# Optimization experiments

Measured on AMD Instinct MI355X. Metric: run time of the kernel, lower is better.

## Reference

```python
import jax, jax.numpy as jnp
import numpy as np

B, Hc, Wc, C, NH, SR, WS = 4, 64, 64, 256, 8, 2, 4
N = Hc * Wc


def _window_partition(x, ws, H, W):
    # x: (B, h, N, d) -> (B*h*nWin, ws*ws, d)
    Bb, h, _, d = x.shape
    x = x.reshape(Bb * h, H // ws, ws, W // ws, ws, d)
    x = x.transpose(0, 1, 3, 2, 4, 5)
    return x.reshape(-1, ws * ws, d)


def _window_reverse(win, ws, H, W, head):
    nwin = (H // ws) * (W // ws)
    Bh = win.shape[0] // nwin
    x = win.reshape(Bh, H // ws, W // ws, ws, ws, -1).transpose(0, 1, 3, 2, 4, 5).reshape(Bh, H, W, -1)
    Bb = Bh // head
    x = x.reshape(Bb, head, H, W, -1).transpose(0, 2, 3, 1, 4)  # heads interleave into channels
    return x.reshape(Bb, H * W, -1)


def _layernorm(x, w, b):
    m = x.mean(-1, keepdims=True)
    v = x.var(-1, keepdims=True)
    return (x - m) / jnp.sqrt(v + 1e-5) * w + b


def setup_inputs() -> dict:
    key = jax.random.key(0)
    ks = jax.random.split(key, 16)
    lin = lambda k, i, o: 0.02 * jax.random.normal(k, (i, o), jnp.float32)
    inp = {
        'x': jax.random.normal(ks[0], (B, N, C), jnp.float32),
        'q1_w': lin(ks[1], C, C // 2), 'q1_b': jnp.zeros((C // 2,), jnp.float32),
        'kv1_w': lin(ks[2], C, C), 'kv1_b': jnp.zeros((C,), jnp.float32),
        'q2_w': lin(ks[3], C, C // 2), 'q2_b': jnp.zeros((C // 2,), jnp.float32),
        'kv2_w': lin(ks[4], C, C), 'kv2_b': jnp.zeros((C,), jnp.float32),
        'lepe_w': lin(ks[5], C, C), 'lepe_b': jnp.zeros((C,), jnp.float32),
        'lepe_conv_w': jnp.sqrt(2.0 / 9.0) * jax.random.normal(ks[6], (C, 1, 3, 3), jnp.float32),
        'lepe_conv_b': jnp.zeros((C,), jnp.float32),
        'sr_w': jnp.sqrt(2.0 / (SR * SR * C)) * jax.random.normal(ks[7], (C, C, SR, SR), jnp.float32),
        'sr_b': jnp.zeros((C,), jnp.float32),
        'norm_w': jnp.ones((C,), jnp.float32), 'norm_b': jnp.zeros((C,), jnp.float32),
        'proj_w': lin(ks[8], C, C), 'proj_b': jnp.zeros((C,), jnp.float32),
        'H': Hc, 'W': Wc,
    }
    return inp


def reference(x, q1_w, q1_b, kv1_w, kv1_b, q2_w, q2_b, kv2_w, kv2_b,
              lepe_w, lepe_b, lepe_conv_w, lepe_conv_b, sr_w, sr_b,
              norm_w, norm_b, proj_w, proj_b, H, W):
    Bb, Nn, Cc = x.shape
    h2 = NH // 2
    d = Cc // NH
    sr = sr_w.shape[-1]
    scale = d ** -0.5
    ws = WS

    # lepe: linear -> depthwise 3x3 conv
    l = (x @ lepe_w + lepe_b).transpose(0, 2, 1).reshape(Bb, Cc, H, W)
    l = jax.lax.conv_general_dilated(l, lepe_conv_w, (1, 1), ((1, 1), (1, 1)),
                                     dimension_numbers=('NCHW', 'OIHW', 'NCHW'),
                                     feature_group_count=Cc) + lepe_conv_b[None, :, None, None]
    lepe = l.reshape(Bb, Cc, Nn).transpose(0, 2, 1)

    # branch 1: spatial-reduction global attention
    q1 = (x @ q1_w + q1_b).reshape(Bb, Nn, h2, d).transpose(0, 2, 1, 3)
    x_img = x.transpose(0, 2, 1).reshape(Bb, Cc, H, W)
    xs = jax.lax.conv_general_dilated(x_img, sr_w, (sr, sr), 'VALID',
                                      dimension_numbers=('NCHW', 'OIHW', 'NCHW')) + sr_b[None, :, None, None]
    N1 = (H // sr) * (W // sr)
    xs = xs.reshape(Bb, Cc, N1).transpose(0, 2, 1)
    xs = jax.nn.gelu(_layernorm(xs, norm_w, norm_b), approximate=False)
    kv1 = (xs @ kv1_w + kv1_b).reshape(Bb, N1, 2, h2, d).transpose(2, 0, 3, 1, 4)
    k1, v1 = kv1[0], kv1[1]
    attn1 = jax.nn.softmax(jnp.einsum('bhnd,bhmd->bhnm', q1, k1) * scale, axis=-1)
    x1 = jnp.einsum('bhnm,bhmd->bnhd', attn1, v1).reshape(Bb, Nn, Cc // 2)
    g = jax.lax.stop_gradient(attn1).mean(1).mean(1).reshape(Bb, H // sr, W // sr)
    g = jnp.repeat(jnp.repeat(g, sr, axis=1), sr, axis=2)  # nearest upsample to (B,H,W)

    # branch 2: Swin-style windowed attention (window 4)
    q2 = (x @ q2_w + q2_b).reshape(Bb, Nn, h2, d).transpose(0, 2, 1, 3)
    kv2 = (x @ kv2_w + kv2_b).reshape(Bb, Nn, 2, h2, d).transpose(2, 0, 3, 1, 4)
    k2, v2 = kv2[0], kv2[1]
    q2w = _window_partition(q2, ws, H, W)
    k2w = _window_partition(k2, ws, H, W)
    v2w = _window_partition(v2, ws, H, W)
    attn2 = jax.nn.softmax(jnp.einsum('wnd,wmd->wnm', q2w, k2w) * scale, axis=-1)
    x2 = jnp.einsum('wnm,wmd->wnd', attn2, v2w)
    x2 = _window_reverse(x2, ws, H, W, h2)
    nwin = (H // ws) * (W // ws)
    lm = jax.lax.stop_gradient(attn2).reshape(Bb, h2, nwin, ws * ws, ws * ws).mean(1).mean(2)
    lm = lm.reshape(Bb, H // ws, W // ws, ws, ws).transpose(0, 1, 3, 2, 4).reshape(Bb, H, W)

    out = jnp.concatenate([x1, x2], axis=-1)
    p = (out + lepe) @ proj_w + proj_b
    out = p + p  # proj_drop is identity at p=0.0, so x = drop(p) + p = 2p

    mask = lm + g
    mask1 = mask.reshape(Bb, H * W)
    mask2 = mask.transpose(0, 2, 1).reshape(Bb, H * W)
    return out, mask1, mask2
```

## Files before the change

kernel.cpp:

```cpp
#include <hip/hip_runtime.h>
#include <hip/hip_bf16.h>
#include <math.h>

typedef __hip_bfloat16 bf16;
typedef __attribute__((ext_vector_type(8))) short bf16x8;
typedef __attribute__((ext_vector_type(4))) short bf16x4;
typedef __attribute__((ext_vector_type(4))) float f32x4;

__device__ __forceinline__ float b2f(bf16 v) { return __bfloat162float(v); }
__device__ __forceinline__ bf16  f2b(float v) { return __float2bfloat16(v); }
__device__ __forceinline__ float s2f(short v) { return __uint_as_float(((unsigned)(unsigned short)v) << 16); }

__global__ void detect_dtype(const void* x, int* flag)
{
    __shared__ int cnt;
    if (threadIdx.x == 0) cnt = 0;
    __syncthreads();
    const unsigned* w = (const unsigned*)x;
    int sane = 0;
    for (int i = threadIdx.x; i < 2048; i += 256) {
        unsigned lo = (w[i] & 0xFFFFu) << 16;
        float v = __uint_as_float(lo);
        float a = fabsf(v);
        if (v == 0.f || (a > 1e-8f && a < 1e4f)) sane++;
    }
    atomicAdd(&cnt, sane);
    __syncthreads();
    if (threadIdx.x == 0) *flag = (cnt < 1640) ? 1 : 0;
}

__global__ void convert_x4(const void* __restrict__ src, bf16* __restrict__ dst,
                           const int* __restrict__ flag)
{
    int i = blockIdx.x * 256 + threadIdx.x;
    bf16 tmp[4];
    if (*flag) {
        float4 v = ((const float4*)src)[i];
        tmp[0] = f2b(v.x); tmp[1] = f2b(v.y); tmp[2] = f2b(v.z); tmp[3] = f2b(v.w);
        *(bf16x4*)&dst[i * 4] = *(bf16x4*)tmp;
    } else {
        ((bf16x4*)dst)[i] = ((const bf16x4*)src)[i];
    }
}

struct PackArgs { const void* src[10]; bf16* dst[10]; int n[10]; };
__global__ void pack_small(PackArgs a, const int* __restrict__ flag)
{
    int bi = blockIdx.x;
    int n = a.n[bi];
    const void* s = a.src[bi];
    bf16* d = a.dst[bi];
    for (int i = threadIdx.x; i < n; i += 256)
        d[i] = (*flag) ? f2b(((const float*)s)[i]) : f2b(s2f(((const short*)s)[i]));
}

struct WTArgs { const void* src[6]; bf16* dst[6]; int N[6]; int blkoff[7]; };
__global__ void convert_wT_multi(WTArgs a, const int* __restrict__ flag)
{
    int blk = blockIdx.x;
    int ti = 0;
    while (blk >= a.blkoff[ti + 1]) ++ti;
    int o = (blk - a.blkoff[ti]) * 256 + threadIdx.x;
    int n = o >> 8, k = o & 255;
    int N = a.N[ti];
    float v = (*flag) ? ((const float*)a.src[ti])[k * N + n]
                      : s2f(((const short*)a.src[ti])[k * N + n]);
    a.dst[ti][o] = f2b(v);
}

__global__ void convert_srwT(const void* __restrict__ src, bf16* __restrict__ dst,
                             const int* __restrict__ flag)
{
    int o = blockIdx.x * 256 + threadIdx.x;
    int co = o >> 10, kg = o & 1023;
    int e = kg >> 8, ci = kg & 255;
    int si = co * 1024 + ci * 4 + e;
    float v = (*flag) ? ((const float*)src)[si] : s2f(((const short*)src)[si]);
    dst[o] = f2b(v);
}

__global__ void convert_dwT(const void* __restrict__ src, bf16* __restrict__ dst,
                            const int* __restrict__ flag)
{
    int o = blockIdx.x * 256 + threadIdx.x;
    if (o >= 2304) return;
    int k = o >> 8, c = o & 255;
    float v = (*flag) ? ((const float*)src)[c * 9 + k] : s2f(((const short*)src)[c * 9 + k]);
    dst[o] = f2b(v);
}

__global__ __launch_bounds__(256) void gemm_qkv128(
    const bf16* __restrict__ A, const bf16* __restrict__ WT, const bf16* __restrict__ bias,
    bf16* __restrict__ Cl, bf16* __restrict__ Cq1, bf16* __restrict__ Cq2, bf16* __restrict__ Ckv2)
{
    __shared__ bf16 As[128][40];
    __shared__ bf16 Bs[128][40];
    int t = threadIdx.x;
    int m0 = blockIdx.x * 128, ybase = blockIdx.y * 128;
    int w = t >> 6, l = t & 63, lane16 = l & 15, quad = l >> 4;
    int wr = w >> 1, wc = w & 1;
    int sr = t >> 1, sc = (t & 1) * 16;
    f32x4 acc[4][4] = {};
    for (int k0 = 0; k0 < 256; k0 += 32) {
        *(bf16x8*)&As[sr][sc]     = *(const bf16x8*)&A[(size_t)(m0 + sr) * 256 + k0 + sc];
        *(bf16x8*)&As[sr][sc + 8] = *(const bf16x8*)&A[(size_t)(m0 + sr) * 256 + k0 + sc + 8];
        *(bf16x8*)&Bs[sr][sc]     = *(const bf16x8*)&WT[(size_t)(ybase + sr) * 256 + k0 + sc];
        *(bf16x8*)&Bs[sr][sc + 8] = *(const bf16x8*)&WT[(size_t)(ybase + sr) * 256 + k0 + sc + 8];
        __syncthreads();
        bf16x8 a[4], b[4];
        #pragma unroll
        for (int i = 0; i < 4; ++i) {
            a[i] = *(const bf16x8*)&As[wr * 64 + i * 16 + lane16][quad * 8];
            b[i] = *(const bf16x8*)&Bs[wc * 64 + i * 16 + lane16][quad * 8];
        }
        #pragma unroll
        for (int i = 0; i < 4; ++i)
            #pragma unroll
            for (int j = 0; j < 4; ++j)
                acc[i][j] = __builtin_amdgcn_mfma_f32_16x16x32_bf16(a[i], b[j], acc[i][j], 0, 0, 0);
        __syncthreads();
    }
    bf16* C; int N, cbase;
    if (ybase < 256)      { C = Cl;   N = 256; cbase = ybase; }
    else if (ybase < 384) { C = Cq1;  N = 128; cbase = ybase - 256; }
    else if (ybase < 512) { C = Cq2;  N = 128; cbase = ybase - 384; }
    else                  { C = Ckv2; N = 256; cbase = ybase - 512; }
    #pragma unroll
    for (int j = 0; j < 4; ++j) {
        int gcol = ybase + wc * 64 + j * 16 + lane16;
        float bv = b2f(bias[gcol]);
        int col = cbase + wc * 64 + j * 16 + lane16;
        #pragma unroll
        for (int i = 0; i < 4; ++i)
            #pragma unroll
            for (int r = 0; r < 4; ++r) {
                int row = m0 + wr * 64 + i * 16 + quad * 4 + r;
                C[(size_t)row * N + col] = f2b(acc[i][j][r] + bv);
            }
    }
}

__global__ __launch_bounds__(256) void gemm_proj128(
    const bf16* __restrict__ A, const bf16* __restrict__ A2,
    const bf16* __restrict__ WT, const bf16* __restrict__ bias,
    void* __restrict__ dout, const int* __restrict__ flag)
{
    __shared__ bf16 As[128][40];
    __shared__ bf16 Bs[128][40];
    int t = threadIdx.x;
    int m0 = blockIdx.x * 128, n0 = blockIdx.y * 128;
    int w = t >> 6, l = t & 63, lane16 = l & 15, quad = l >> 4;
    int wr = w >> 1, wc = w & 1;
    int sr = t >> 1, sc = (t & 1) * 16;
    f32x4 acc[4][4] = {};
    for (int k0 = 0; k0 < 256; k0 += 32) {
        #pragma unroll
        for (int hh = 0; hh < 2; ++hh) {
            bf16x8 va = *(const bf16x8*)&A[(size_t)(m0 + sr) * 256 + k0 + sc + hh * 8];
            bf16x8 vb = *(const bf16x8*)&A2[(size_t)(m0 + sr) * 256 + k0 + sc + hh * 8];
            bf16 tmp[8];
            #pragma unroll
            for (int q = 0; q < 8; ++q) tmp[q] = f2b(s2f(va[q]) + s2f(vb[q]));
            *(bf16x8*)&As[sr][sc + hh * 8] = *(bf16x8*)tmp;
        }
        *(bf16x8*)&Bs[sr][sc]     = *(const bf16x8*)&WT[(size_t)(n0 + sr) * 256 + k0 + sc];
        *(bf16x8*)&Bs[sr][sc + 8] = *(const bf16x8*)&WT[(size_t)(n0 + sr) * 256 + k0 + sc + 8];
        __syncthreads();
        bf16x8 a[4], b[4];
        #pragma unroll
        for (int i = 0; i < 4; ++i) {
            a[i] = *(const bf16x8*)&As[wr * 64 + i * 16 + lane16][quad * 8];
            b[i] = *(const bf16x8*)&Bs[wc * 64 + i * 16 + lane16][quad * 8];
        }
        #pragma unroll
        for (int i = 0; i < 4; ++i)
            #pragma unroll
            for (int j = 0; j < 4; ++j)
                acc[i][j] = __builtin_amdgcn_mfma_f32_16x16x32_bf16(a[i], b[j], acc[i][j], 0, 0, 0);
        __syncthreads();
    }
    #pragma unroll
    for (int j = 0; j < 4; ++j) {
        int col = n0 + wc * 64 + j * 16 + lane16;
        float bv = b2f(bias[col]);
        #pragma unroll
        for (int i = 0; i < 4; ++i)
            #pragma unroll
            for (int r = 0; r < 4; ++r) {
                int row = m0 + wr * 64 + i * 16 + quad * 4 + r;
                float rv = (acc[i][j][r] + bv) * 2.f;
                size_t o = (size_t)row * 256 + col;
                if (*flag) ((float*)dout)[o] = rv;
                else       ((bf16*)dout)[o] = f2b(rv);
            }
    }
}

__global__ __launch_bounds__(256) void gemm_sr_mfma(
    const bf16* __restrict__ x, const bf16* __restrict__ WT,
    const bf16* __restrict__ bias, bf16* __restrict__ C)
{
    __shared__ bf16 As[64][40];
    __shared__ bf16 Bs[64][40];
    int t = threadIdx.x;
    int m0 = blockIdx.x * 64, n0 = blockIdx.y * 64;
    int w = t >> 6, l = t & 63, lane16 = l & 15, quad = l >> 4;
    int sr = t >> 2, sc = (t & 3) * 8;
    int brow = m0 + sr;
    int b = brow >> 10, p = brow & 1023;
    int pi = p >> 5, pj = p & 31;
    f32x4 acc[4] = {};
    for (int k0 = 0; k0 < 1024; k0 += 32) {
        int kg = k0 + sc;
        int e = kg >> 8, ci = kg & 255;
        int di = e >> 1, dj = e & 1;
        int n = (2 * pi + di) * 64 + 2 * pj + dj;
        *(bf16x8*)&As[sr][sc] = *(const bf16x8*)&x[(size_t)((b << 12) + n) * 256 + ci];
        *(bf16x8*)&Bs[sr][sc] = *(const bf16x8*)&WT[(size_t)(n0 + sr) * 1024 + kg];
        __syncthreads();
        bf16x8 a = *(const bf16x8*)&As[w * 16 + lane16][quad * 8];
        #pragma unroll
        for (int ct = 0; ct < 4; ++ct) {
            bf16x8 bb = *(const bf16x8*)&Bs[ct * 16 + lane16][quad * 8];
            acc[ct] = __builtin_amdgcn_mfma_f32_16x16x32_bf16(a, bb, acc[ct], 0, 0, 0);
        }
        __syncthreads();
    }
    #pragma unroll
    for (int ct = 0; ct < 4; ++ct) {
        int col = n0 + ct * 16 + lane16;
        float bv = b2f(bias[col]);
        #pragma unroll
        for (int r = 0; r < 4; ++r) {
            int row = m0 + w * 16 + quad * 4 + r;
            C[(size_t)row * 256 + col] = f2b(acc[ct][r] + bv);
        }
    }
}

__global__ __launch_bounds__(256) void gemm_kv1(
    const bf16* __restrict__ A, const bf16* __restrict__ WT, const bf16* __restrict__ bias,
    bf16* __restrict__ k1, bf16* __restrict__ v1T)
{
    __shared__ bf16 As[64][40];
    __shared__ bf16 Bs[64][40];
    int t = threadIdx.x;
    int m0 = blockIdx.x * 64, n0 = blockIdx.y * 64;
    int w = t >> 6, l = t & 63, lane16 = l & 15, quad = l >> 4;
    int sr = t >> 2, sc = (t & 3) * 8;
    f32x4 acc[4] = {};
    for (int k0 = 0; k0 < 256; k0 += 32) {
        *(bf16x8*)&As[sr][sc] = *(const bf16x8*)&A[(size_t)(m0 + sr) * 256 + k0 + sc];
        *(bf16x8*)&Bs[sr][sc] = *(const bf16x8*)&WT[(size_t)(n0 + sr) * 256 + k0 + sc];
        __syncthreads();
        bf16x8 a = *(const bf16x8*)&As[w * 16 + lane16][quad * 8];
        #pragma unroll
        for (int ct = 0; ct < 4; ++ct) {
            bf16x8 b = *(const bf16x8*)&Bs[ct * 16 + lane16][quad * 8];
            acc[ct] = __builtin_amdgcn_mfma_f32_16x16x32_bf16(a, b, acc[ct], 0, 0, 0);
        }
        __syncthreads();
    }
    #pragma unroll
    for (int ct = 0; ct < 4; ++ct) {
        int col = n0 + ct * 16 + lane16;
        float bv = b2f(bias[col]);
        #pragma unroll
        for (int r = 0; r < 4; ++r) {
            int row = m0 + w * 16 + quad * 4 + r;
            float val = acc[ct][r] + bv;
            int bb = row >> 10, key = row & 1023;
            if (col < 128) {
                k1[(size_t)row * 128 + col] = f2b(val);
            } else {
                int h = (col - 128) >> 5, ch = (col - 128) & 31;
                v1T[(size_t)((bb * 4 + h) * 32 + ch) * 1024 + key] = f2b(val);
            }
        }
    }
}

__global__ __launch_bounds__(256) void dwconv3v(
    const bf16* __restrict__ lin, const bf16* __restrict__ dwT,
    const bf16* __restrict__ bias, bf16* __restrict__ out)
{
    int tid = blockIdx.x * 256 + threadIdx.x;
    int c0 = (tid & 31) * 8;
    int n = (tid >> 5) & 4095;
    int b = tid >> 17;
    int i = n >> 6, j = n & 63;
    float acc[8];
    bf16x8 bv = *(const bf16x8*)&bias[c0];
    #pragma unroll
    for (int q = 0; q < 8; ++q) acc[q] = s2f(bv[q]);
    #pragma unroll
    for (int di = 0; di < 3; ++di) {
        int ii = i + di - 1;
        if (ii < 0 || ii > 63) continue;
        #pragma unroll
        for (int dj = 0; dj < 3; ++dj) {
            int jj = j + dj - 1;
            if (jj < 0 || jj > 63) continue;
            bf16x8 xv = *(const bf16x8*)&lin[(size_t)((b << 12) + ii * 64 + jj) * 256 + c0];
            bf16x8 wv = *(const bf16x8*)&dwT[(di * 3 + dj) * 256 + c0];
            #pragma unroll
            for (int q = 0; q < 8; ++q) acc[q] += s2f(xv[q]) * s2f(wv[q]);
        }
    }
    bf16 ov[8];
    #pragma unroll
    for (int q = 0; q < 8; ++q) ov[q] = f2b(acc[q]);
    *(bf16x8*)&out[(size_t)((b << 12) + n) * 256 + c0] = *(bf16x8*)ov;
}

__global__ __launch_bounds__(256) void ln_gelu_w(
    const bf16* __restrict__ xin, const bf16* __restrict__ nw,
    const bf16* __restrict__ nb, bf16* __restrict__ xout)
{
    int w = threadIdx.x >> 6, lane = threadIdx.x & 63;
    int r = blockIdx.x * 4 + w;
    bf16x4 xv = *(const bf16x4*)&xin[(size_t)r * 256 + lane * 4];
    float v[4];
    #pragma unroll
    for (int j = 0; j < 4; ++j) v[j] = s2f(xv[j]);
    float s = v[0] + v[1] + v[2] + v[3];
    #pragma unroll
    for (int o = 1; o <= 32; o <<= 1) s += __shfl_xor(s, o);
    float mean = s * (1.f / 256.f);
    float ss = 0.f;
    #pragma unroll
    for (int j = 0; j < 4; ++j) { float d = v[j] - mean; ss += d * d; }
    #pragma unroll
    for (int o = 1; o <= 32; o <<= 1) ss += __shfl_xor(ss, o);
    float inv = rsqrtf(ss * (1.f / 256.f) + 1e-5f);
    bf16x4 wv = *(const bf16x4*)&nw[lane * 4];
    bf16x4 bv = *(const bf16x4*)&nb[lane * 4];
    bf16 ov[4];
    #pragma unroll
    for (int j = 0; j < 4; ++j) {
        float y = (v[j] - mean) * inv * s2f(wv[j]) + s2f(bv[j]);
        ov[j] = f2b(0.5f * y * (1.f + erff(y * 0.70710678118654752f)));
    }
    *(bf16x4*)&xout[(size_t)r * 256 + lane * 4] = *(bf16x4*)ov;
}

__global__ __launch_bounds__(256) void attn1_mfma3(
    const bf16* __restrict__ q1, const bf16* __restrict__ k1,
    const bf16* __restrict__ v1T, bf16* __restrict__ attn_out, float* __restrict__ g)
{
    __shared__ bf16 PTT[4][16][72];
    __shared__ float gp[1024];

    int t = threadIdx.x;
    int blk = blockIdx.x;
    int qc = blk & 63, h = (blk >> 6) & 3, b = blk >> 8;
    int n0 = qc * 64;
    int w = t >> 6, l = t & 63, lane16 = l & 15, quad = l >> 4;
    const float scale = 0.17677669529663687f;

    const bf16* Kbase = k1 + (size_t)b * 1024 * 128 + 32 * h;
    const bf16* Vbase = v1T + (size_t)((b * 4 + h) * 32) * 1024;
    bf16x8 qa = *(const bf16x8*)&q1[(size_t)(b * 4096 + n0 + 16 * w + lane16) * 128 + 32 * h + quad * 8];

    for (int i = t; i < 1024; i += 256) gp[i] = 0.f;
    __syncthreads();

    bf16* ptt = &PTT[w][0][0];
    float lacc = 0.f;
    f32x4 oT0 = {}, oT1 = {};

    for (int kt = 0; kt < 16; ++kt) {
        bf16x8 kf[4];
        #pragma unroll
        for (int st = 0; st < 4; ++st)
            kf[st] = *(const bf16x8*)&Kbase[(size_t)(kt * 64 + st * 16 + lane16) * 128 + quad * 8];
        bf16x8 vf[2][2];
        #pragma unroll
        for (int ct = 0; ct < 2; ++ct)
            #pragma unroll
            for (int kh = 0; kh < 2; ++kh)
                vf[ct][kh] = *(const bf16x8*)&Vbase[(size_t)(ct * 16 + lane16) * 1024 + kt * 64 + kh * 32 + quad * 8];
        #pragma unroll
        for (int st = 0; st < 4; ++st) {
            f32x4 z = {0.f, 0.f, 0.f, 0.f};
            f32x4 sT = __builtin_amdgcn_mfma_f32_16x16x32_bf16(kf[st], qa, z, 0, 0, 0);
            bf16 pk[4];
            #pragma unroll
            for (int r = 0; r < 4; ++r) {
                float p = __expf(sT[r] * scale);
                lacc += p;
                pk[r] = f2b(p);
            }
            *(bf16x4*)&ptt[lane16 * 72 + st * 16 + quad * 4] = *(bf16x4*)pk;
        }
        #pragma unroll
        for (int kh = 0; kh < 2; ++kh) {
            bf16x8 pf = *(const bf16x8*)&ptt[lane16 * 72 + kh * 32 + quad * 8];
            oT0 = __builtin_amdgcn_mfma_f32_16x16x32_bf16(vf[0][kh], pf, oT0, 0, 0, 0);
            oT1 = __builtin_amdgcn_mfma_f32_16x16x32_bf16(vf[1][kh], pf, oT1, 0, 0, 0);
        }
    }
    lacc += __shfl_xor(lacc, 16);
    lacc += __shfl_xor(lacc, 32);
    float rl = 1.f / lacc;
    float rlq[4];
    #pragma unroll
    for (int r = 0; r < 4; ++r) rlq[r] = __shfl(rl, quad * 4 + r);

    for (int kt = 0; kt < 16; ++kt) {
        #pragma unroll
        for (int st = 0; st < 4; ++st) {
            bf16x8 kf = *(const bf16x8*)&Kbase[(size_t)(kt * 64 + st * 16 + lane16) * 128 + quad * 8];
            f32x4 z = {0.f, 0.f, 0.f, 0.f};
            f32x4 s = __builtin_amdgcn_mfma_f32_16x16x32_bf16(qa, kf, z, 0, 0, 0);
            float cs = 0.f;
            #pragma unroll
            for (int r = 0; r < 4; ++r) cs += __expf(s[r] * scale) * rlq[r];
            cs += __shfl_xor(cs, 16);
            cs += __shfl_xor(cs, 32);
            if (quad == 0) atomicAdd(&gp[kt * 64 + st * 16 + lane16], cs);
        }
    }

    #pragma unroll
    for (int ct = 0; ct < 2; ++ct) {
        f32x4 o = ct ? oT1 : oT0;
        bf16 ov[4];
        #pragma unroll
        for (int r = 0; r < 4; ++r) ov[r] = f2b(o[r] * rl);
        *(bf16x4*)&attn_out[(size_t)(b * 4096 + n0 + 16 * w + lane16) * 256 + 32 * h + ct * 16 + quad * 4] = *(bf16x4*)ov;
    }
    __syncthreads();
    for (int i = t; i < 1024; i += 256)
        atomicAdd(&g[(b << 10) + i], gp[i] * (1.f / 16384.f));
}

__global__ __launch_bounds__(64) void attn2_vec(
    const bf16* __restrict__ q2, const bf16* __restrict__ kv2,
    bf16* __restrict__ attn_out, float* __restrict__ lm)
{
    __shared__ float P2[64][17];
    int t = threadIdx.x;
    int blk = blockIdx.x;
    int b = blk >> 8, win = blk & 255;
    int wi = win >> 4, wj = win & 15;
    int h = t >> 4, qi = t & 15;
    int nq = (wi * 4 + (qi >> 2)) * 64 + wj * 4 + (qi & 3);

    float qv[32];
    {
        const bf16* qp = q2 + (size_t)(b * 4096 + nq) * 128 + h * 32;
        #pragma unroll
        for (int g8 = 0; g8 < 4; ++g8) {
            bf16x8 v = *(const bf16x8*)&qp[g8 * 8];
            #pragma unroll
            for (int j = 0; j < 8; ++j) qv[g8 * 8 + j] = s2f(v[j]) * 0.17677669529663687f;
        }
    }
    float s[16];
    float mx = -1e30f;
    #pragma unroll
    for (int k = 0; k < 16; ++k) {
        int nk = (wi * 4 + (k >> 2)) * 64 + wj * 4 + (k & 3);
        const bf16* kp = kv2 + (size_t)(b * 4096 + nk) * 256 + h * 32;
        float ss = 0.f;
        #pragma unroll
        for (int g8 = 0; g8 < 4; ++g8) {
            bf16x8 v = *(const bf16x8*)&kp[g8 * 8];
            #pragma unroll
            for (int j = 0; j < 8; ++j) ss += qv[g8 * 8 + j] * s2f(v[j]);
        }
        s[k] = ss;
        mx = fmaxf(mx, ss);
    }
    float lsum = 0.f;
    #pragma unroll
    for (int k = 0; k < 16; ++k) { s[k] = __expf(s[k] - mx); lsum += s[k]; }
    float rl = 1.f / lsum;
    #pragma unroll
    for (int k = 0; k < 16; ++k) s[k] *= rl;

    float o[32];
    #pragma unroll
    for (int d = 0; d < 32; ++d) o[d] = 0.f;
    #pragma unroll
    for (int k = 0; k < 16; ++k) {
        int nk = (wi * 4 + (k >> 2)) * 64 + wj * 4 + (k & 3);
        const bf16* vp = kv2 + (size_t)(b * 4096 + nk) * 256 + 128 + h * 32;
        float p = s[k];
        #pragma unroll
        for (int g8 = 0; g8 < 4; ++g8) {
            bf16x8 v = *(const bf16x8*)&vp[g8 * 8];
            #pragma unroll
            for (int j = 0; j < 8; ++j) o[g8 * 8 + j] += p * s2f(v[j]);
        }
    }
    {
        bf16* op = attn_out + (size_t)(b * 4096 + nq) * 256 + 128 + h * 32;
        #pragma unroll
        for (int g8 = 0; g8 < 4; ++g8) {
            bf16 ov[8];
            #pragma unroll
            for (int j = 0; j < 8; ++j) ov[j] = f2b(o[g8 * 8 + j]);
            *(bf16x8*)&op[g8 * 8] = *(bf16x8*)ov;
        }
    }

    #pragma unroll
    for (int k = 0; k < 16; ++k) P2[t][k] = s[k];
    __syncthreads();
    if (t < 16) {
        float cs = 0.f;
        for (int qq = 0; qq < 64; ++qq) cs += P2[qq][t];
        int nk = (wi * 4 + (t >> 2)) * 64 + wj * 4 + (t & 3);
        lm[(b << 12) + nk] = cs * (1.f / 64.f);
    }
}

__global__ void mask_combine(const float* __restrict__ lm, const float* __restrict__ g,
                             void* __restrict__ dout, const int* __restrict__ flag)
{
    int tid = blockIdx.x * 256 + threadIdx.x;
    int b = tid >> 12, n = tid & 4095;
    int i = n >> 6, j = n & 63;
    float v = lm[tid] + g[(b << 10) + (i >> 1) * 32 + (j >> 1)];
    size_t o1 = (size_t)4194304 + (b << 12) + i * 64 + j;
    size_t o2 = (size_t)4194304 + 16384 + (b << 12) + j * 64 + i;
    if (*flag) { ((float*)dout)[o1] = v; ((float*)dout)[o2] = v; }
    else       { ((bf16*)dout)[o1] = f2b(v); ((bf16*)dout)[o2] = f2b(v); }
}

extern "C" void kernel_launch(void* const* d_in, const int* in_sizes, int n_in,
                              void* d_out, int out_size, void* d_ws, size_t ws_size,
                              hipStream_t stream)
{
    char* ws = (char*)d_ws;
    size_t off = 0;
    auto alloc = [&](size_t bytes) {
        void* p = ws + off;
        off += (bytes + 255) & ~(size_t)255;
        return p;
    };
    bf16* cx       = (bf16*)alloc((size_t)4194304 * 2);
    bf16* lepe_lin = (bf16*)alloc((size_t)4194304 * 2);
    bf16* attn_out = lepe_lin;
    bf16* lepe     = (bf16*)alloc((size_t)4194304 * 2);
    bf16* q1buf    = (bf16*)alloc((size_t)2097152 * 2);
    bf16* q2buf    = (bf16*)alloc((size_t)2097152 * 2);
    bf16* kv2buf   = (bf16*)alloc((size_t)4194304 * 2);
    bf16* xs_pre   = (bf16*)alloc((size_t)1048576 * 2);
    bf16* k1buf    = xs_pre;
    bf16* v1Tbuf   = xs_pre + 524288;
    bf16* xs       = (bf16*)alloc((size_t)1048576 * 2);
    bf16* wTqkv    = (bf16*)alloc((size_t)196608 * 2);
    bf16* kv1_wT   = (bf16*)alloc(65536 * 2);
    bf16* proj_wT  = (bf16*)alloc(65536 * 2);
    bf16* sr_wT    = (bf16*)alloc(262144 * 2);
    bf16* dwT      = (bf16*)alloc(2304 * 2);
    bf16* bcat     = (bf16*)alloc(768 * 2);
    bf16* ckv1b    = (bf16*)alloc(256 * 2);
    bf16* csrb     = (bf16*)alloc(256 * 2);
    bf16* cnw      = (bf16*)alloc(256 * 2);
    bf16* cnb      = (bf16*)alloc(256 * 2);
    bf16* cpb      = (bf16*)alloc(256 * 2);
    bf16* clcb     = (bf16*)alloc(256 * 2);
    float* gbuf    = (float*)alloc(4096 * 4);
    float* lmbuf   = (float*)alloc(16384 * 4);
    int*   flag    = (int*)alloc(256);

    detect_dtype<<<1, 256, 0, stream>>>(d_in[0], flag);

    convert_x4<<<4096, 256, 0, stream>>>(d_in[0], cx, flag);

    PackArgs pa;
    pa.src[0] = d_in[10]; pa.dst[0] = bcat;       pa.n[0] = 256;
    pa.src[1] = d_in[2];  pa.dst[1] = bcat + 256; pa.n[1] = 128;
    pa.src[2] = d_in[6];  pa.dst[2] = bcat + 384; pa.n[2] = 128;
    pa.src[3] = d_in[8];  pa.dst[3] = bcat + 512; pa.n[3] = 256;
    pa.src[4] = d_in[4];  pa.dst[4] = ckv1b;      pa.n[4] = 256;
    pa.src[5] = d_in[14]; pa.dst[5] = csrb;       pa.n[5] = 256;
    pa.src[6] = d_in[15]; pa.dst[6] = cnw;        pa.n[6] = 256;
    pa.src[7] = d_in[16]; pa.dst[7] = cnb;        pa.n[7] = 256;
    pa.src[8] = d_in[18]; pa.dst[8] = cpb;        pa.n[8] = 256;
    pa.src[9] = d_in[12]; pa.dst[9] = clcb;       pa.n[9] = 256;
    pack_small<<<10, 256, 0, stream>>>(pa, flag);

    WTArgs wa;
    wa.src[0] = d_in[9];  wa.dst[0] = wTqkv;             wa.N[0] = 256;
    wa.src[1] = d_in[1];  wa.dst[1] = wTqkv + 256 * 256; wa.N[1] = 128;
    wa.src[2] = d_in[5];  wa.dst[2] = wTqkv + 384 * 256; wa.N[2] = 128;
    wa.src[3] = d_in[7];  wa.dst[3] = wTqkv + 512 * 256; wa.N[3] = 256;
    wa.src[4] = d_in[3];  wa.dst[4] = kv1_wT;            wa.N[4] = 256;
    wa.src[5] = d_in[17]; wa.dst[5] = proj_wT;           wa.N[5] = 256;
    int bo[7] = {0, 256, 384, 512, 768, 1024, 1280};
    for (int i = 0; i < 7; ++i) wa.blkoff[i] = bo[i];
    convert_wT_multi<<<1280, 256, 0, stream>>>(wa, flag);

    convert_srwT<<<1024, 256, 0, stream>>>(d_in[13], sr_wT, flag);
    convert_dwT<<<9, 256, 0, stream>>>(d_in[11], dwT, flag);

    hipMemsetAsync(gbuf, 0, 4096 * 4, stream);

    gemm_qkv128<<<dim3(128, 6), 256, 0, stream>>>(cx, wTqkv, bcat, lepe_lin, q1buf, q2buf, kv2buf);
    gemm_sr_mfma<<<dim3(64, 4), 256, 0, stream>>>(cx, sr_wT, csrb, xs_pre);
    ln_gelu_w<<<1024, 256, 0, stream>>>(xs_pre, cnw, cnb, xs);
    gemm_kv1<<<dim3(64, 4), 256, 0, stream>>>(xs, kv1_wT, ckv1b, k1buf, v1Tbuf);
    dwconv3v<<<2048, 256, 0, stream>>>(lepe_lin, dwT, clcb, lepe);
    attn1_mfma3<<<1024, 256, 0, stream>>>(q1buf, k1buf, v1Tbuf, attn_out, gbuf);
    attn2_vec<<<1024, 64, 0, stream>>>(q2buf, kv2buf, attn_out, lmbuf);
    gemm_proj128<<<dim3(128, 2), 256, 0, stream>>>(attn_out, lepe, proj_wT, cpb, d_out, flag);
    mask_combine<<<64, 256, 0, stream>>>(lmbuf, gbuf, d_out, flag);
}
```

Baseline: 297.9 us.

## Split attn1 key range across two wave groups and stage K/V in LDS

The branch-1 attention kernel now uses 512 threads per block. Two groups of four waves each process half of the 1024 keys, and their partial softmax sums and outputs are merged through shared memory. K and V tiles are staged cooperatively into LDS instead of each wave loading them directly from global memory. The aim is more waves in flight and shorter serial key loops per wave, at the cost of extra barriers, a larger LDS footprint and a cross-group reduction step.

```diff
diff --git a/kernel.cpp b/kernel.cpp
--- a/kernel.cpp
+++ b/kernel.cpp
@@ -344,46 +344,49 @@
     *(bf16x4*)&xout[(size_t)r * 256 + lane * 4] = *(bf16x4*)ov;
 }
 
-__global__ __launch_bounds__(256) void attn1_mfma3(
+__global__ __launch_bounds__(512) void attn1_split(
     const bf16* __restrict__ q1, const bf16* __restrict__ k1,
     const bf16* __restrict__ v1T, bf16* __restrict__ attn_out, float* __restrict__ g)
 {
-    __shared__ bf16 PTT[4][16][72];
+    __shared__ bf16 Kt[2][64][40];
+    __shared__ bf16 Vt[2][32][68];
+    __shared__ bf16 PTT[8][16][72];
     __shared__ float gp[1024];
+    __shared__ float Lcmb[4][16];
+    __shared__ float rls[4][16];
+    __shared__ __align__(16) float Ocmb[4][16][36];
 
     int t = threadIdx.x;
     int blk = blockIdx.x;
     int qc = blk & 63, h = (blk >> 6) & 3, b = blk >> 8;
     int n0 = qc * 64;
     int w = t >> 6, l = t & 63, lane16 = l & 15, quad = l >> 4;
+    int grp = w >> 2, qg = w & 3;
+    int tg = t & 255;
     const float scale = 0.17677669529663687f;
 
-    const bf16* Kbase = k1 + (size_t)b * 1024 * 128 + 32 * h;
-    const bf16* Vbase = v1T + (size_t)((b * 4 + h) * 32) * 1024;
-    bf16x8 qa = *(const bf16x8*)&q1[(size_t)(b * 4096 + n0 + 16 * w + lane16) * 128 + 32 * h + quad * 8];
-
-    for (int i = t; i < 1024; i += 256) gp[i] = 0.f;
-    __syncthreads();
-
+    const bf16* Kbase = k1 + (size_t)b * 1024 * 128 + 32 * h + (size_t)(grp * 512) * 128;
+    const bf16* Vbase = v1T + (size_t)((b * 4 + h) * 32) * 1024 + grp * 512;
+    bf16x8 qa = *(const bf16x8*)&q1[(size_t)(b * 4096 + n0 + 16 * qg + lane16) * 128 + 32 * h + quad * 8];
+
+    for (int i = t; i < 1024; i += 512) gp[i] = 0.f;
+
+    int sr = tg >> 2, sc = (tg & 3) * 8;
+    int vrow = tg >> 3, vcol = (tg & 7) * 8;
     bf16* ptt = &PTT[w][0][0];
+
     float lacc = 0.f;
     f32x4 oT0 = {}, oT1 = {};
 
-    for (int kt = 0; kt < 16; ++kt) {
-        bf16x8 kf[4];
-        #pragma unroll
-        for (int st = 0; st < 4; ++st)
-            kf[st] = *(const bf16x8*)&Kbase[(size_t)(kt * 64 + st * 16 + lane16) * 128 + quad * 8];
-        bf16x8 vf[2][2];
-        #pragma unroll
-        for (int ct = 0; ct < 2; ++ct)
-            #pragma unroll
-            for (int kh = 0; kh < 2; ++kh)
-                vf[ct][kh] = *(const bf16x8*)&Vbase[(size_t)(ct * 16 + lane16) * 1024 + kt * 64 + kh * 32 + quad * 8];
+    for (int ktl = 0; ktl < 8; ++ktl) {
+        *(bf16x8*)&Kt[grp][sr][sc] = *(const bf16x8*)&Kbase[(size_t)(ktl * 64 + sr) * 128 + sc];
+        *(bf16x8*)&Vt[grp][vrow][vcol] = *(const bf16x8*)&Vbase[(size_t)vrow * 1024 + ktl * 64 + vcol];
+        __syncthreads();
         #pragma unroll
         for (int st = 0; st < 4; ++st) {
+            bf16x8 kf = *(const bf16x8*)&Kt[grp][st * 16 + lane16][quad * 8];
             f32x4 z = {0.f, 0.f, 0.f, 0.f};
-            f32x4 sT = __builtin_amdgcn_mfma_f32_16x16x32_bf16(kf[st], qa, z, 0, 0, 0);
+            f32x4 sT = __builtin_amdgcn_mfma_f32_16x16x32_bf16(kf, qa, z, 0, 0, 0);
             bf16 pk[4];
             #pragma unroll
             for (int r = 0; r < 4; ++r) {
@@ -396,21 +399,52 @@
         #pragma unroll
         for (int kh = 0; kh < 2; ++kh) {
             bf16x8 pf = *(const bf16x8*)&ptt[lane16 * 72 + kh * 32 + quad * 8];
-            oT0 = __builtin_amdgcn_mfma_f32_16x16x32_bf16(vf[0][kh], pf, oT0, 0, 0, 0);
-            oT1 = __builtin_amdgcn_mfma_f32_16x16x32_bf16(vf[1][kh], pf, oT1, 0, 0, 0);
-        }
-    }
+            bf16x8 vf0 = *(const bf16x8*)&Vt[grp][lane16][kh * 32 + quad * 8];
+            bf16x8 vf1 = *(const bf16x8*)&Vt[grp][16 + lane16][kh * 32 + quad * 8];
+            oT0 = __builtin_amdgcn_mfma_f32_16x16x32_bf16(vf0, pf, oT0, 0, 0, 0);
+            oT1 = __builtin_amdgcn_mfma_f32_16x16x32_bf16(vf1, pf, oT1, 0, 0, 0);
+        }
+        __syncthreads();
+    }
+
     lacc += __shfl_xor(lacc, 16);
     lacc += __shfl_xor(lacc, 32);
-    float rl = 1.f / lacc;
+
+    if (grp == 1) {
+        if (quad == 0) Lcmb[qg][lane16] = lacc;
+        *(f32x4*)&Ocmb[qg][lane16][quad * 4]      = oT0;
+        *(f32x4*)&Ocmb[qg][lane16][16 + quad * 4] = oT1;
+    }
+    __syncthreads();
+    if (grp == 0) {
+        float ltot = lacc + Lcmb[qg][lane16];
+        float rl = 1.f / ltot;
+        if (quad == 0) rls[qg][lane16] = rl;
+        f32x4 p0 = *(const f32x4*)&Ocmb[qg][lane16][quad * 4];
+        f32x4 p1 = *(const f32x4*)&Ocmb[qg][lane16][16 + quad * 4];
+        bf16 ov0[4], ov1[4];
+        #pragma unroll
+        for (int r = 0; r < 4; ++r) {
+            ov0[r] = f2b((oT0[r] + p0[r]) * rl);
+            ov1[r] = f2b((oT1[r] + p1[r]) * rl);
+        }
+        size_t ro = (size_t)(b * 4096 + n0 + 16 * qg + lane16) * 256 + 32 * h;
+        *(bf16x4*)&attn_out[ro + quad * 4]      = *(bf16x4*)ov0;
+        *(bf16x4*)&attn_out[ro + 16 + quad * 4] = *(bf16x4*)ov1;
+    }
+    __syncthreads();
+
     float rlq[4];
     #pragma unroll
-    for (int r = 0; r < 4; ++r) rlq[r] = __shfl(rl, quad * 4 + r);
-
-    for (int kt = 0; kt < 16; ++kt) {
+    for (int r = 0; r < 4; ++r) rlq[r] = rls[qg][quad * 4 + r];
+
+    int sr2 = tg >> 2, sc2 = (tg & 3) * 8;
+    for (int ktl = 0; ktl < 8; ++ktl) {
+        *(bf16x8*)&Kt[grp][sr2][sc2] = *(const bf16x8*)&Kbase[(size_t)(ktl * 64 + sr2) * 128 + sc2];
+        __syncthreads();
         #pragma unroll
         for (int st = 0; st < 4; ++st) {
-            bf16x8 kf = *(const bf16x8*)&Kbase[(size_t)(kt * 64 + st * 16 + lane16) * 128 + quad * 8];
+            bf16x8 kf = *(const bf16x8*)&Kt[grp][st * 16 + lane16][quad * 8];
             f32x4 z = {0.f, 0.f, 0.f, 0.f};
             f32x4 s = __builtin_amdgcn_mfma_f32_16x16x32_bf16(qa, kf, z, 0, 0, 0);
             float cs = 0.f;
@@ -418,20 +452,12 @@
             for (int r = 0; r < 4; ++r) cs += __expf(s[r] * scale) * rlq[r];
             cs += __shfl_xor(cs, 16);
             cs += __shfl_xor(cs, 32);
-            if (quad == 0) atomicAdd(&gp[kt * 64 + st * 16 + lane16], cs);
-        }
-    }
-
-    #pragma unroll
-    for (int ct = 0; ct < 2; ++ct) {
-        f32x4 o = ct ? oT1 : oT0;
-        bf16 ov[4];
-        #pragma unroll
-        for (int r = 0; r < 4; ++r) ov[r] = f2b(o[r] * rl);
-        *(bf16x4*)&attn_out[(size_t)(b * 4096 + n0 + 16 * w + lane16) * 256 + 32 * h + ct * 16 + quad * 4] = *(bf16x4*)ov;
-    }
-    __syncthreads();
-    for (int i = t; i < 1024; i += 256)
+            if (quad == 0) atomicAdd(&gp[grp * 512 + ktl * 64 + st * 16 + lane16], cs);
+        }
+        __syncthreads();
+    }
+
+    for (int i = t; i < 1024; i += 512)
         atomicAdd(&g[(b << 10) + i], gp[i] * (1.f / 16384.f));
 }
 
@@ -606,7 +632,7 @@
     ln_gelu_w<<<1024, 256, 0, stream>>>(xs_pre, cnw, cnb, xs);
     gemm_kv1<<<dim3(64, 4), 256, 0, stream>>>(xs, kv1_wT, ckv1b, k1buf, v1Tbuf);
     dwconv3v<<<2048, 256, 0, stream>>>(lepe_lin, dwT, clcb, lepe);
-    attn1_mfma3<<<1024, 256, 0, stream>>>(q1buf, k1buf, v1Tbuf, attn_out, gbuf);
+    attn1_split<<<1024, 512, 0, stream>>>(q1buf, k1buf, v1Tbuf, attn_out, gbuf);
     attn2_vec<<<1024, 64, 0, stream>>>(q2buf, kv2buf, attn_out, lmbuf);
     gemm_proj128<<<dim3(128, 2), 256, 0, stream>>>(attn_out, lepe, proj_wT, cpb, d_out, flag);
     mask_combine<<<64, 256, 0, stream>>>(lmbuf, gbuf, d_out, flag);
```

After: 268.3 us. 1.11x faster.
